# Performance work log

Hardware: AMD Instinct MI355X
Metric: run time of the kernel (lower is better)

Reference implementation:

```python
import jax, jax.numpy as jnp
import numpy as np

EMB_DIM = 512
QKV_DIM = 512
NUM_HEADS = 8
HEAD_DIM = QKV_DIM // NUM_HEADS
NUM_LANDMARKS = 64
N_ITER = 6


def setup_inputs() -> dict:
    key = jax.random.key(0)
    ks = jax.random.split(key, 9)
    s = 1.0 / np.sqrt(EMB_DIM)
    return {
        "x": jax.random.normal(ks[0], (4, 8192, EMB_DIM), dtype=jnp.float32),
        "Wq": jax.random.normal(ks[1], (EMB_DIM, QKV_DIM), dtype=jnp.float32) * s,
        "bq": jnp.zeros((QKV_DIM,), dtype=jnp.float32),
        "Wk": jax.random.normal(ks[2], (EMB_DIM, QKV_DIM), dtype=jnp.float32) * s,
        "bk": jnp.zeros((QKV_DIM,), dtype=jnp.float32),
        "Wv": jax.random.normal(ks[3], (EMB_DIM, QKV_DIM), dtype=jnp.float32) * s,
        "bv": jnp.zeros((QKV_DIM,), dtype=jnp.float32),
        "Wo": jax.random.normal(ks[4], (QKV_DIM, EMB_DIM), dtype=jnp.float32) * s,
        "bo": jnp.zeros((EMB_DIM,), dtype=jnp.float32),
    }


def _split_heads(x):
    bs, sl, _ = x.shape
    return x.reshape(bs, sl, NUM_HEADS, HEAD_DIM).transpose(0, 2, 1, 3)


def _iterative_inv(K):
    # K: [bs, h, L, L]; Newton-Schulz pseudo-inverse, 'original' init
    L = K.shape[-1]
    I = jnp.eye(L, dtype=K.dtype)
    V = K.swapaxes(-1, -2) / jnp.max(jnp.sum(K, axis=-2))
    for _ in range(N_ITER):
        KV = jnp.matmul(K, V)
        V = jnp.matmul(0.25 * V, 13.0 * I - jnp.matmul(KV, 15.0 * I - jnp.matmul(KV, 7.0 * I - KV)))
    return V


def reference(x, Wq, bq, Wk, bk, Wv, bv, Wo, bo):
    bs, seqlen, _ = x.shape
    # seqlen chosen divisible by NUM_LANDMARKS, so no padding branch
    full_len = seqlen
    q = _split_heads(x @ Wq + bq)
    k = _split_heads(x @ Wk + bk)
    v = _split_heads(x @ Wv + bv)
    scale = 1.0 / np.sqrt(np.sqrt(HEAD_DIM))
    q = q * scale
    k = k * scale

    seg = full_len // NUM_LANDMARKS
    q_land = q.reshape(bs, NUM_HEADS, NUM_LANDMARKS, seg, HEAD_DIM).mean(axis=-2)
    k_land = k.reshape(bs, NUM_HEADS, NUM_LANDMARKS, seg, HEAD_DIM).mean(axis=-2)

    kernel_1 = jax.nn.softmax(jnp.einsum('bhsd,bhld->bhsl', q, k_land), axis=-1)  # [bs,h,S,L]
    kernel_2 = jax.nn.softmax(jnp.einsum('bhld,bhmd->bhlm', q_land, k_land), axis=-1)  # [bs,h,L,L]
    kernel_3 = jax.nn.softmax(jnp.einsum('bhld,bhsd->bhls', q_land, k), axis=-1)  # [bs,h,L,S]

    out = jnp.matmul(jnp.matmul(kernel_1, _iterative_inv(kernel_2)), jnp.matmul(kernel_3, v))  # [bs,h,S,d]
    out = out.transpose(0, 2, 1, 3).reshape(bs, seqlen, QKV_DIM)
    return out @ Wo + bo
```

## Files before the change

### kernel.cpp

```cpp
#include <hip/hip_runtime.h>

#define BS 4
#define SEQL 8192
#define EMB 512
#define NH 8
#define HD 64
#define LM 64
#define SEG 128
#define BH (BS*NH)
#define NCH 16
#define CHS (SEQL/NCH)
#define QSCALE 0.35355339059327373f

typedef unsigned short u16;
typedef __bf16 bf16_t;
typedef __attribute__((ext_vector_type(8))) __bf16 bf16x8;
typedef __attribute__((ext_vector_type(4))) float f32x4;

#define MFMA16(a, b, c) __builtin_amdgcn_mfma_f32_16x16x32_bf16((a), (b), (c), 0, 0, 0)

__device__ __forceinline__ float bf2f(u16 u) {
  return __uint_as_float(((unsigned int)u) << 16);
}
__device__ __forceinline__ u16 f2bf(float f) {
  unsigned int u = __float_as_uint(f);
  u += 0x7fffu + ((u >> 16) & 1u);
  return (u16)(u >> 16);
}
__device__ __forceinline__ float load1_any(const void* p, size_t idx, int isf32) {
  return isf32 ? ((const float*)p)[idx] : bf2f(((const u16*)p)[idx]);
}
__device__ __forceinline__ void load4_any(const void* p, size_t idx, int isf32, float* dst) {
  if (isf32) {
    float4 v = *reinterpret_cast<const float4*>((const float*)p + idx);
    dst[0] = v.x; dst[1] = v.y; dst[2] = v.z; dst[3] = v.w;
  } else {
    ushort4 v = *reinterpret_cast<const ushort4*>((const u16*)p + idx);
    dst[0] = bf2f(v.x); dst[1] = bf2f(v.y); dst[2] = bf2f(v.z); dst[3] = bf2f(v.w);
  }
}
__device__ __forceinline__ void ld8_bf(const void* p, size_t idx, int isf32, u16* o) {
  if (isf32) {
    const float* f = (const float*)p + idx;
    float4 a = *reinterpret_cast<const float4*>(f);
    float4 b = *reinterpret_cast<const float4*>(f + 4);
    o[0] = f2bf(a.x); o[1] = f2bf(a.y); o[2] = f2bf(a.z); o[3] = f2bf(a.w);
    o[4] = f2bf(b.x); o[5] = f2bf(b.y); o[6] = f2bf(b.z); o[7] = f2bf(b.w);
  } else {
    *reinterpret_cast<int4*>(o) = *reinterpret_cast<const int4*>((const u16*)p + idx);
  }
}

__device__ __forceinline__ void async16(const void* g, void* l) {
  __builtin_amdgcn_global_load_lds(
      (const __attribute__((address_space(1))) void*)g,
      (__attribute__((address_space(3))) void*)l, 16, 0, 0);
}

__global__ __launch_bounds__(256) void probe_kernel(const void* x, int* flag) {
  __shared__ int cnt;
  if (threadIdx.x == 0) cnt = 0;
  __syncthreads();
  const u16* p = (const u16*)x;
  int c = 0;
  for (int j = 0; j < 16; j++) {
    u16 u = p[(size_t)(threadIdx.x * 16 + j) * 2];
    int e = (u >> 7) & 0xFF;
    if (e >= 134) c++;
  }
  atomicAdd(&cnt, c);
  __syncthreads();
  if (threadIdx.x == 0) flag[0] = (cnt > 256) ? 1 : 0;
}

__global__ __launch_bounds__(256) void prep_wt_kernel(
    const void* Wq, const void* Wk, const void* Wv, const void* Wo, const int* flag,
    u16* __restrict__ WqT, u16* __restrict__ WkT, u16* __restrict__ WvT, u16* __restrict__ WoT)
{
  __shared__ u16 Ws[64 * 72];
  const int id = blockIdx.x;
  const int z = id >> 6, tile = id & 63;
  const int k0 = (tile >> 3) * 64, n0 = (tile & 7) * 64;
  const void* W = (z == 0) ? Wq : (z == 1) ? Wk : (z == 2) ? Wv : Wo;
  u16* WT = (z == 0) ? WqT : (z == 1) ? WkT : (z == 2) ? WvT : WoT;
  const int isf32 = flag[0];
  const int t = threadIdx.x;
  const int r = t >> 2, cq = (t & 3) * 16;
  u16 tmp[8];
  #pragma unroll
  for (int u = 0; u < 2; u++) {
    ld8_bf(W, (size_t)(k0 + r) * EMB + n0 + cq + 8 * u, isf32, tmp);
    *reinterpret_cast<int4*>(&Ws[r * 72 + cq + 8 * u]) = *reinterpret_cast<int4*>(tmp);
  }
  __syncthreads();
  const int nn = t >> 2, kq = (t & 3) * 16;
  #pragma unroll
  for (int u = 0; u < 2; u++) {
    u16 o[8];
    #pragma unroll
    for (int j = 0; j < 8; j++) o[j] = Ws[(kq + 8 * u + j) * 72 + nn];
    *reinterpret_cast<int4*>(&WT[(size_t)(n0 + nn) * EMB + k0 + kq + 8 * u]) =
        *reinterpret_cast<int4*>(o);
  }
}

__global__ __launch_bounds__(256) void xmean_kernel(const void* x, const int* flag,
                                                    float* __restrict__ xmean) {
  const int bl = blockIdx.x;
  const int t = threadIdx.x;
  const int isf32 = flag[0];
  const int c = t * 2;
  const size_t base = (size_t)bl * SEG * EMB;
  float s0 = 0.f, s1 = 0.f;
  for (int r = 0; r < SEG; r++) {
    size_t idx = base + (size_t)r * EMB + c;
    if (isf32) {
      float2 v = *reinterpret_cast<const float2*>((const float*)x + idx);
      s0 += v.x; s1 += v.y;
    } else {
      ushort2 v = *reinterpret_cast<const ushort2*>((const u16*)x + idx);
      s0 += bf2f(v.x); s1 += bf2f(v.y);
    }
  }
  xmean[(size_t)bl * EMB + c]     = s0 * (1.0f / SEG);
  xmean[(size_t)bl * EMB + c + 1] = s1 * (1.0f / SEG);
}

__global__ __launch_bounds__(256) void lm_proj_kernel(
    const float* __restrict__ xmean,
    const void* Wq, const void* bq, const void* Wk, const void* bk,
    const int* flag, float* __restrict__ qL, float* __restrict__ kL,
    u16* __restrict__ qLb, u16* __restrict__ kLb)
{
  __shared__ float As[64 * 17];
  __shared__ float Bs[16 * 64];
  const int t = threadIdx.x;
  const int m0 = blockIdx.x * 64, n0 = blockIdx.y * 64, z = blockIdx.z;
  const void* W    = z ? Wk : Wq;
  const void* bias = z ? bk : bq;
  float* dst       = z ? kL : qL;
  u16*   dstb      = z ? kLb : qLb;
  const int isf32 = flag[0];
  const int tx = t & 15, ty = t >> 4;
  const int arow = t >> 2, akk = (t & 3) << 2;
  const int brow = t >> 4, bcol = (t & 15) << 2;
  float acc[4][4] = {};
  for (int k0 = 0; k0 < EMB; k0 += 16) {
    float4 av = *reinterpret_cast<const float4*>(xmean + (size_t)(m0 + arow) * EMB + k0 + akk);
    As[arow * 17 + akk + 0] = av.x;
    As[arow * 17 + akk + 1] = av.y;
    As[arow * 17 + akk + 2] = av.z;
    As[arow * 17 + akk + 3] = av.w;
    load4_any(W, (size_t)(k0 + brow) * EMB + n0 + bcol, isf32, &Bs[brow * 64 + bcol]);
    __syncthreads();
    #pragma unroll
    for (int kk = 0; kk < 16; kk++) {
      float a[4], b[4];
      #pragma unroll
      for (int i = 0; i < 4; i++) a[i] = As[(ty * 4 + i) * 17 + kk];
      #pragma unroll
      for (int j = 0; j < 4; j++) b[j] = Bs[kk * 64 + tx * 4 + j];
      #pragma unroll
      for (int i = 0; i < 4; i++)
        #pragma unroll
        for (int j = 0; j < 4; j++)
          acc[i][j] = fmaf(a[i], b[j], acc[i][j]);
    }
    __syncthreads();
  }
  #pragma unroll
  for (int i = 0; i < 4; i++) {
    int m = m0 + ty * 4 + i;
    int b = m >> 6, l = m & 63;
    #pragma unroll
    for (int j = 0; j < 4; j++) {
      int n = n0 + tx * 4 + j;
      int h = n >> 6, d = n & 63;
      float c = (acc[i][j] + load1_any(bias, n, isf32)) * QSCALE;
      size_t idx = (size_t)((b * NH + h) * LM + l) * HD + d;
      dst[idx] = c;
      dstb[idx] = f2bf(c);
    }
  }
}

__global__ __launch_bounds__(256, 3) void proj_qkv_fused_kernel(
    const void* x, const u16* __restrict__ WqT, const u16* __restrict__ WkT,
    const u16* __restrict__ WvT,
    const void* bq, const void* bk, const void* bv, const int* flag,
    u16* __restrict__ Qb, u16* __restrict__ Kb, u16* __restrict__ VbT)
{
  __shared__ u16 smem[128 * 72 + 3 * 64 * 64];
  u16* As = smem;
  u16* Bs = smem + 128 * 72;
  const int t = threadIdx.x;
  const int orig = blockIdx.x;
  const int swz  = (orig & 7) * 256 + (orig >> 3);
  const int h    = swz & 7;
  const int m0   = (swz >> 3) * 128;
  const int n0   = h * 64;
  const int isf32 = flag[0];
  const int w = t >> 6, lane = t & 63, q = lane >> 4, c = lane & 15;
  const int wm = (w >> 1) * 64, wn = (w & 1) * 32;
  const int sr = t >> 1, sh = (t & 1) * 32;
  const int brow8 = lane >> 3;
  const int bsw   = ((lane & 7) ^ brow8) * 8;

  f32x4 acc[3][4][2];
  f32x4 z4 = {0.f, 0.f, 0.f, 0.f};
  #pragma unroll
  for (int z = 0; z < 3; z++)
    #pragma unroll
    for (int mi = 0; mi < 4; mi++) { acc[z][mi][0] = z4; acc[z][mi][1] = z4; }

  for (int k0 = 0; k0 < EMB; k0 += 64) {
    __syncthreads();
    #pragma unroll
    for (int u = 0; u < 6; u++) {
      int cb = u * 4 + w;
      int z = cb >> 3, r8 = cb & 7;
      const u16* Wt = (z == 0) ? WqT : (z == 1) ? WkT : WvT;
      async16(&Wt[(size_t)(n0 + r8 * 8 + brow8) * EMB + k0 + bsw],
              &Bs[z * 4096 + r8 * 512]);
    }
    u16 tmp[8];
    #pragma unroll
    for (int u = 0; u < 4; u++) {
      ld8_bf(x, (size_t)(m0 + sr) * EMB + k0 + sh + 8 * u, isf32, tmp);
      *reinterpret_cast<int4*>(&As[sr * 72 + sh + 8 * u]) = *reinterpret_cast<int4*>(tmp);
    }
    __syncthreads();
    #pragma unroll
    for (int kk = 0; kk < 64; kk += 32) {
      bf16x8 af[4];
      #pragma unroll
      for (int mi = 0; mi < 4; mi++)
        af[mi] = *reinterpret_cast<const bf16x8*>(&As[(wm + mi * 16 + c) * 72 + kk + q * 8]);
      const int u0 = ((((kk >> 3) + q) ^ (c & 7))) * 8;
      #pragma unroll
      for (int z = 0; z < 3; z++) {
        bf16x8 b0 = *reinterpret_cast<const bf16x8*>(&Bs[z * 4096 + (wn + c) * 64 + u0]);
        bf16x8 b1 = *reinterpret_cast<const bf16x8*>(&Bs[z * 4096 + (wn + 16 + c) * 64 + u0]);
        #pragma unroll
        for (int mi = 0; mi < 4; mi++) {
          acc[z][mi][0] = MFMA16(af[mi], b0, acc[z][mi][0]);
          acc[z][mi][1] = MFMA16(af[mi], b1, acc[z][mi][1]);
        }
      }
    }
  }

  float bb[3][2];
  #pragma unroll
  for (int z = 0; z < 3; z++) {
    const void* bias = (z == 0) ? bq : (z == 1) ? bk : bv;
    bb[z][0] = load1_any(bias, n0 + wn + c, isf32);
    bb[z][1] = load1_any(bias, n0 + wn + 16 + c, isf32);
  }
  const int b = m0 >> 13, s0t = m0 & (SEQL - 1);

  #pragma unroll
  for (int z = 0; z < 2; z++) {
    u16* dst = z ? Kb : Qb;
    #pragma unroll
    for (int mi = 0; mi < 4; mi++)
      #pragma unroll
      for (int i = 0; i < 4; i++) {
        int s = s0t + wm + mi * 16 + q * 4 + i;
        size_t rowb = ((size_t)((b * NH + h) * SEQL + s)) * HD;
        dst[rowb + wn + c]      = f2bf((acc[z][mi][0][i] + bb[z][0]) * QSCALE);
        dst[rowb + wn + 16 + c] = f2bf((acc[z][mi][1][i] + bb[z][1]) * QSCALE);
      }
  }

  __syncthreads();
  #pragma unroll
  for (int mi = 0; mi < 4; mi++)
    #pragma unroll
    for (int i = 0; i < 4; i++) {
      int ml = wm + mi * 16 + q * 4 + i;
      smem[(wn + c) * 136 + ml]      = f2bf(acc[2][mi][0][i] + bb[2][0]);
      smem[(wn + 16 + c) * 136 + ml] = f2bf(acc[2][mi][1][i] + bb[2][1]);
    }
  __syncthreads();
  const int nl = t >> 2, cq2 = (t & 3) * 32;
  #pragma unroll
  for (int u = 0; u < 4; u++)
    *reinterpret_cast<int4*>(&VbT[((size_t)((b * NH + h) * HD + nl)) * SEQL + s0t + cq2 + 8 * u]) =
        *reinterpret_cast<int4*>(&smem[nl * 136 + cq2 + 8 * u]);
}

__global__ __launch_bounds__(256) void k2_softmax_kernel(
    const float* __restrict__ qL, const float* __restrict__ kL,
    float* __restrict__ K2, float* __restrict__ cs)
{
  __shared__ float qs[64 * 65], ks[64 * 65], ps[64 * 65];
  const int t = threadIdx.x, bh = blockIdx.x;
  const int r = t >> 2, cb = (t & 3) << 4;
  #pragma unroll
  for (int i = 0; i < 16; i++) {
    qs[r * 65 + cb + i] = qL[((size_t)bh * LM + r) * HD + cb + i];
    ks[r * 65 + cb + i] = kL[((size_t)bh * LM + r) * HD + cb + i];
  }
  __syncthreads();
  float lg[16] = {};
  for (int d = 0; d < HD; d++) {
    float a = qs[r * 65 + d];
    #pragma unroll
    for (int i = 0; i < 16; i++) lg[i] = fmaf(a, ks[(cb + i) * 65 + d], lg[i]);
  }
  float m = lg[0];
  #pragma unroll
  for (int i = 1; i < 16; i++) m = fmaxf(m, lg[i]);
  m = fmaxf(m, __shfl_xor(m, 1));
  m = fmaxf(m, __shfl_xor(m, 2));
  float s = 0.f;
  #pragma unroll
  for (int i = 0; i < 16; i++) { lg[i] = __expf(lg[i] - m); s += lg[i]; }
  s += __shfl_xor(s, 1);
  s += __shfl_xor(s, 2);
  const float inv = 1.0f / s;
  #pragma unroll
  for (int i = 0; i < 16; i++) {
    float p = lg[i] * inv;
    ps[r * 65 + cb + i] = p;
    K2[((size_t)bh * LM + r) * LM + cb + i] = p;
  }
  __syncthreads();
  if (t < 64) {
    float c = 0.f;
    for (int rr = 0; rr < 64; rr++) c += ps[rr * 65 + t];
    cs[bh * LM + t] = c;
  }
}

__device__ __forceinline__ void mm_split(const u16* Ah, const u16* Al,
                                         const u16* Bh, const u16* Bl,
                                         int w, int lane, f32x4* out)
{
  const int q = lane >> 4, c = lane & 15;
  bf16x8 ah[2], al[2];
  #pragma unroll
  for (int k2 = 0; k2 < 2; k2++) {
    ah[k2] = *reinterpret_cast<const bf16x8*>(&Ah[(w * 16 + c) * 72 + k2 * 32 + q * 8]);
    al[k2] = *reinterpret_cast<const bf16x8*>(&Al[(w * 16 + c) * 72 + k2 * 32 + q * 8]);
  }
  #pragma unroll
  for (int nb = 0; nb < 4; nb++) {
    f32x4 acc = {0.f, 0.f, 0.f, 0.f};
    #pragma unroll
    for (int k2 = 0; k2 < 2; k2++) {
      bf16x8 bh_ = *reinterpret_cast<const bf16x8*>(&Bh[(nb * 16 + c) * 72 + k2 * 32 + q * 8]);
      bf16x8 bl_ = *reinterpret_cast<const bf16x8*>(&Bl[(nb * 16 + c) * 72 + k2 * 32 + q * 8]);
      acc = MFMA16(ah[k2], bh_, acc);
      acc = MFMA16(ah[k2], bl_, acc);
      acc = MFMA16(al[k2], bh_, acc);
    }
    out[nb] = acc;
  }
}

__global__ __launch_bounds__(256) void ns_inverse_kernel(
    const float* __restrict__ K2, const float* __restrict__ cs,
    float* __restrict__ Vi)
{
  __shared__ u16 K2h[64 * 72], K2l[64 * 72];
  __shared__ u16 VAh[64 * 72], VAl[64 * 72];
  __shared__ u16 VTh[64 * 72], VTl[64 * 72];
  __shared__ u16 KVh[64 * 72], KVl[64 * 72];
  __shared__ u16 Th [64 * 72], Tl [64 * 72];
  __shared__ float red[256];
  const int t = threadIdx.x, bh = blockIdx.x;
  const int w = t >> 6, lane = t & 63, q = lane >> 4, c = lane & 15;

  float m = -1e30f;
  for (int i = t; i < BH * LM; i += 256) m = fmaxf(m, cs[i]);
  red[t] = m;
  __syncthreads();
  for (int off = 128; off; off >>= 1) {
    if (t < off) red[t] = fmaxf(red[t], red[t + off]);
    __syncthreads();
  }
  const float ginv = 1.0f / red[0];
  __syncthreads();

  {
    const int r = t >> 2, cb = (t & 3) << 4;
    #pragma unroll
    for (int i = 0; i < 16; i++) {
      float v = K2[((size_t)bh * LM + r) * LM + cb + i];
      u16 h1 = f2bf(v);
      K2h[r * 72 + cb + i] = h1;
      K2l[r * 72 + cb + i] = f2bf(v - bf2f(h1));
      float sv = v * ginv;
      u16 h2 = f2bf(sv);
      u16 l2 = f2bf(sv - bf2f(h2));
      VTh[r * 72 + cb + i] = h2;
      VTl[r * 72 + cb + i] = l2;
      VAh[(cb + i) * 72 + r] = h2;
      VAl[(cb + i) * 72 + r] = l2;
    }
  }
  __syncthreads();

  f32x4 o[4];
  for (int it = 0; it < 6; it++) {
    mm_split(K2h, K2l, VTh, VTl, w, lane, o);
    __syncthreads();
    #pragma unroll
    for (int nb = 0; nb < 4; nb++)
      #pragma unroll
      for (int i = 0; i < 4; i++) {
        const int row = w * 16 + q * 4 + i, col = nb * 16 + c;
        const float v = o[nb][i];
        const u16 h1 = f2bf(v);
        KVh[row * 72 + col] = h1;
        KVl[row * 72 + col] = f2bf(v - bf2f(h1));
        const float tv = (row == col ? 7.0f : 0.0f) - v;
        const u16 h2 = f2bf(tv);
        Th[col * 72 + row] = h2;
        Tl[col * 72 + row] = f2bf(tv - bf2f(h2));
      }
    __syncthreads();
    mm_split(KVh, KVl, Th, Tl, w, lane, o);
    __syncthreads();
    #pragma unroll
    for (int nb = 0; nb < 4; nb++)
      #pragma unroll
      for (int i = 0; i < 4; i++) {
        const int row = w * 16 + q * 4 + i, col = nb * 16 + c;
        const float tv = (row == col ? 15.0f : 0.0f) - o[nb][i];
        const u16 h2 = f2bf(tv);
        Th[col * 72 + row] = h2;
        Tl[col * 72 + row] = f2bf(tv - bf2f(h2));
      }
    __syncthreads();
    mm_split(KVh, KVl, Th, Tl, w, lane, o);
    __syncthreads();
    #pragma unroll
    for (int nb = 0; nb < 4; nb++)
      #pragma unroll
      for (int i = 0; i < 4; i++) {
        const int row = w * 16 + q * 4 + i, col = nb * 16 + c;
        const float tv = (row == col ? 13.0f : 0.0f) - o[nb][i];
        const u16 h2 = f2bf(tv);
        Th[col * 72 + row] = h2;
        Tl[col * 72 + row] = f2bf(tv - bf2f(h2));
      }
    __syncthreads();
    mm_split(VAh, VAl, Th, Tl, w, lane, o);
    __syncthreads();
    #pragma unroll
    for (int nb = 0; nb < 4; nb++)
      #pragma unroll
      for (int i = 0; i < 4; i++) {
        const int row = w * 16 + q * 4 + i, col = nb * 16 + c;
        const float v = 0.25f * o[nb][i];
        const u16 h1 = f2bf(v);
        const u16 l1 = f2bf(v - bf2f(h1));
        VAh[row * 72 + col] = h1;
        VAl[row * 72 + col] = l1;
        VTh[col * 72 + row] = h1;
        VTl[col * 72 + row] = l1;
        if (it == 5) Vi[((size_t)bh * LM + row) * LM + col] = v;
      }
    __syncthreads();
  }
}

__global__ __launch_bounds__(256) void k3v_kernel(
    const u16* __restrict__ qLb, const u16* __restrict__ Kb, const u16* __restrict__ VbT,
    float* __restrict__ pnum, float* __restrict__ pden)
{
  __shared__ u16 Ks[64 * 72], Vs[64 * 72], Ps[64 * 72];
  __shared__ float denL[256];
  const int t = threadIdx.x, ch = blockIdx.x, bh = blockIdx.y;
  const int w = t >> 6, lane = t & 63, q = lane >> 4, c = lane & 15;
  const int sr = t >> 2, sp = (t & 3) * 16;

  bf16x8 aq[4][2];
  #pragma unroll
  for (int mi = 0; mi < 4; mi++)
    #pragma unroll
    for (int k2 = 0; k2 < 2; k2++)
      aq[mi][k2] = *reinterpret_cast<const bf16x8*>(
          &qLb[((size_t)bh * LM + mi * 16 + c) * HD + k2 * 32 + q * 8]);

  f32x4 z4 = {0.f, 0.f, 0.f, 0.f};
  f32x4 nacc[4];
  #pragma unroll
  for (int mi = 0; mi < 4; mi++) nacc[mi] = z4;
  float denr[16] = {};

  for (int sub = 0; sub < 8; sub++) {
    const int s0 = ch * CHS + sub * 64;
    __syncthreads();
    #pragma unroll
    for (int u = 0; u < 2; u++) {
      *reinterpret_cast<int4*>(&Ks[sr * 72 + sp + 8 * u]) =
          *reinterpret_cast<const int4*>(&Kb[((size_t)bh * SEQL + s0 + sr) * HD + sp + 8 * u]);
      *reinterpret_cast<int4*>(&Vs[sr * 72 + sp + 8 * u]) =
          *reinterpret_cast<const int4*>(&VbT[((size_t)(bh * HD + sr)) * SEQL + s0 + sp + 8 * u]);
    }
    __syncthreads();
    f32x4 sacc[4];
    #pragma unroll
    for (int mi = 0; mi < 4; mi++) sacc[mi] = z4;
    bf16x8 bk0 = *reinterpret_cast<const bf16x8*>(&Ks[(w * 16 + c) * 72 + q * 8]);
    bf16x8 bk1 = *reinterpret_cast<const bf16x8*>(&Ks[(w * 16 + c) * 72 + 32 + q * 8]);
    #pragma unroll
    for (int mi = 0; mi < 4; mi++) {
      sacc[mi] = MFMA16(aq[mi][0], bk0, sacc[mi]);
      sacc[mi] = MFMA16(aq[mi][1], bk1, sacc[mi]);
    }
    #pragma unroll
    for (int mi = 0; mi < 4; mi++)
      #pragma unroll
      for (int i = 0; i < 4; i++) {
        float p = __expf(sacc[mi][i]);
        denr[mi * 4 + i] += p;
        Ps[(mi * 16 + q * 4 + i) * 72 + w * 16 + c] = f2bf(p);
      }
    __syncthreads();
    #pragma unroll
    for (int k2 = 0; k2 < 2; k2++) {
      bf16x8 bv_ = *reinterpret_cast<const bf16x8*>(&Vs[(w * 16 + c) * 72 + k2 * 32 + q * 8]);
      #pragma unroll
      for (int mi = 0; mi < 4; mi++) {
        bf16x8 ap = *reinterpret_cast<const bf16x8*>(&Ps[(mi * 16 + c) * 72 + k2 * 32 + q * 8]);
        nacc[mi] = MFMA16(ap, bv_, nacc[mi]);
      }
    }
  }
  #pragma unroll
  for (int mi = 0; mi < 4; mi++)
    #pragma unroll
    for (int i = 0; i < 4; i++)
      pnum[(((size_t)bh * NCH + ch) * LM + mi * 16 + q * 4 + i) * HD + w * 16 + c] = nacc[mi][i];
  #pragma unroll
  for (int v = 0; v < 16; v++) {
    denr[v] += __shfl_xor(denr[v], 1);
    denr[v] += __shfl_xor(denr[v], 2);
    denr[v] += __shfl_xor(denr[v], 4);
    denr[v] += __shfl_xor(denr[v], 8);
  }
  if (c == 0) {
    #pragma unroll
    for (int mi = 0; mi < 4; mi++)
      #pragma unroll
      for (int i = 0; i < 4; i++)
        denL[w * 64 + mi * 16 + q * 4 + i] = denr[mi * 4 + i];
  }
  __syncthreads();
  if (t < 64)
    pden[((size_t)bh * NCH + ch) * LM + t] = denL[t] + denL[64 + t] + denL[128 + t] + denL[192 + t];
}

__global__ __launch_bounds__(256) void k3v_w2_kernel(
    const float* __restrict__ pnum, const float* __restrict__ pden,
    const float* __restrict__ Vi, u16* __restrict__ W2T)
{
  __shared__ float Vs[64 * 65], Ms[64 * 65], den[64];
  const int t = threadIdx.x, bh = blockIdx.x;
  const int r = t >> 2, cb = (t & 3) << 4;
  #pragma unroll
  for (int i = 0; i < 16; i++) Vs[r * 65 + cb + i] = Vi[((size_t)bh * LM + r) * LM + cb + i];
  float acc[16] = {};
  for (int ch = 0; ch < NCH; ch++) {
    const float* p = pnum + (((size_t)bh * NCH + ch) * LM + r) * HD + cb;
    #pragma unroll
    for (int i = 0; i < 16; i++) acc[i] += p[i];
  }
  if ((t & 3) == 0) {
    float d = 0.f;
    for (int ch = 0; ch < NCH; ch++) d += pden[((size_t)bh * NCH + ch) * LM + r];
    den[r] = d;
  }
  __syncthreads();
  const float dinv = 1.0f / den[r];
  #pragma unroll
  for (int i = 0; i < 16; i++) Ms[r * 65 + cb + i] = acc[i] * dinv;
  __syncthreads();
  float o[16] = {};
  for (int k = 0; k < 64; k++) {
    float a = Vs[r * 65 + k];
    #pragma unroll
    for (int i = 0; i < 16; i++) o[i] = fmaf(a, Ms[k * 65 + cb + i], o[i]);
  }
  #pragma unroll
  for (int i = 0; i < 16; i++)
    W2T[((size_t)bh * HD + cb + i) * LM + r] = f2bf(o[i]);
}

__global__ __launch_bounds__(256) void final_kernel(
    const u16* __restrict__ Qb, const u16* __restrict__ kLb, const u16* __restrict__ W2T,
    u16* __restrict__ pre)
{
  __shared__ u16 Ps[64 * 72];
  __shared__ float mxL[256], smL[256];
  const int t = threadIdx.x, st = blockIdx.x, bh = blockIdx.y;
  const int w = t >> 6, lane = t & 63, q = lane >> 4, c = lane & 15;
  const int sb = st * 64;

  bf16x8 aq[4][2], bkL[2], bw2[2];
  #pragma unroll
  for (int mi = 0; mi < 4; mi++)
    #pragma unroll
    for (int k2 = 0; k2 < 2; k2++)
      aq[mi][k2] = *reinterpret_cast<const bf16x8*>(
          &Qb[((size_t)bh * SEQL + sb + mi * 16 + c) * HD + k2 * 32 + q * 8]);
  #pragma unroll
  for (int k2 = 0; k2 < 2; k2++) {
    bkL[k2] = *reinterpret_cast<const bf16x8*>(
        &kLb[((size_t)bh * LM + w * 16 + c) * HD + k2 * 32 + q * 8]);
    bw2[k2] = *reinterpret_cast<const bf16x8*>(
        &W2T[((size_t)bh * HD + w * 16 + c) * LM + k2 * 32 + q * 8]);
  }

  f32x4 z4 = {0.f, 0.f, 0.f, 0.f};
  f32x4 sacc[4];
  #pragma unroll
  for (int mi = 0; mi < 4; mi++) sacc[mi] = z4;
  #pragma unroll
  for (int k2 = 0; k2 < 2; k2++)
    #pragma unroll
    for (int mi = 0; mi < 4; mi++)
      sacc[mi] = MFMA16(aq[mi][k2], bkL[k2], sacc[mi]);

  float mx[16];
  #pragma unroll
  for (int v = 0; v < 16; v++) {
    mx[v] = sacc[v >> 2][v & 3];
    mx[v] = fmaxf(mx[v], __shfl_xor(mx[v], 1));
    mx[v] = fmaxf(mx[v], __shfl_xor(mx[v], 2));
    mx[v] = fmaxf(mx[v], __shfl_xor(mx[v], 4));
    mx[v] = fmaxf(mx[v], __shfl_xor(mx[v], 8));
  }
  if (c == 0) {
    #pragma unroll
    for (int mi = 0; mi < 4; mi++)
      #pragma unroll
      for (int i = 0; i < 4; i++)
        mxL[w * 64 + mi * 16 + q * 4 + i] = mx[mi * 4 + i];
  }
  __syncthreads();
  float p[16], dn[16];
  #pragma unroll
  for (int mi = 0; mi < 4; mi++)
    #pragma unroll
    for (int i = 0; i < 4; i++) {
      int row = mi * 16 + q * 4 + i;
      float M = fmaxf(fmaxf(mxL[row], mxL[64 + row]), fmaxf(mxL[128 + row], mxL[192 + row]));
      float pp = __expf(sacc[mi][i] - M);
      p[mi * 4 + i] = pp;
      dn[mi * 4 + i] = pp;
    }
  #pragma unroll
  for (int v = 0; v < 16; v++) {
    dn[v] += __shfl_xor(dn[v], 1);
    dn[v] += __shfl_xor(dn[v], 2);
    dn[v] += __shfl_xor(dn[v], 4);
    dn[v] += __shfl_xor(dn[v], 8);
  }
  if (c == 0) {
    #pragma unroll
    for (int mi = 0; mi < 4; mi++)
      #pragma unroll
      for (int i = 0; i < 4; i++)
        smL[w * 64 + mi * 16 + q * 4 + i] = dn[mi * 4 + i];
  }
  #pragma unroll
  for (int mi = 0; mi < 4; mi++)
    #pragma unroll
    for (int i = 0; i < 4; i++)
      Ps[(mi * 16 + q * 4 + i) * 72 + w * 16 + c] = f2bf(p[mi * 4 + i]);
  __syncthreads();

  f32x4 oacc[4];
  #pragma unroll
  for (int mi = 0; mi < 4; mi++) oacc[mi] = z4;
  #pragma unroll
  for (int k2 = 0; k2 < 2; k2++)
    #pragma unroll
    for (int mi = 0; mi < 4; mi++) {
      bf16x8 ap = *reinterpret_cast<const bf16x8*>(&Ps[(mi * 16 + c) * 72 + k2 * 32 + q * 8]);
      oacc[mi] = MFMA16(ap, bw2[k2], oacc[mi]);
    }
  #pragma unroll
  for (int mi = 0; mi < 4; mi++)
    #pragma unroll
    for (int i = 0; i < 4; i++) {
      int row = mi * 16 + q * 4 + i;
      float den = smL[row] + smL[64 + row] + smL[128 + row] + smL[192 + row];
      float v = oacc[mi][i] / den;
      pre[((size_t)((bh >> 3) * SEQL + sb + row)) * EMB + (bh & 7) * HD + w * 16 + c] = f2bf(v);
    }
}

__global__ __launch_bounds__(256, 3) void out_proj_kernel(
    const u16* __restrict__ pre, const u16* __restrict__ WoT, const void* bo,
    const int* flag, void* out)
{
  __shared__ u16 As[128 * 64];
  __shared__ u16 Bs[128 * 64];
  const int t = threadIdx.x;
  const int m0 = blockIdx.x * 128, n0 = blockIdx.y * 128;
  const int isf32 = flag[0];
  const int w = t >> 6, lane = t & 63, q = lane >> 4, c = lane & 15;
  const int wm = (w >> 1) * 64, wn = (w & 1) * 64;
  const int row8 = lane >> 3;
  const int colsw = ((lane & 7) ^ row8) * 8;

  f32x4 acc[4][4];
  f32x4 z4 = {0.f, 0.f, 0.f, 0.f};
  #pragma unroll
  for (int mi = 0; mi < 4; mi++)
    #pragma unroll
    for (int ni = 0; ni < 4; ni++) acc[mi][ni] = z4;

  for (int k0 = 0; k0 < EMB; k0 += 64) {
    __syncthreads();
    #pragma unroll
    for (int u = 0; u < 4; u++) {
      int chA = u * 4 + w;
      async16(&pre[(size_t)(m0 + chA * 8 + row8) * EMB + k0 + colsw], &As[chA * 512]);
      async16(&WoT[(size_t)(n0 + chA * 8 + row8) * EMB + k0 + colsw], &Bs[chA * 512]);
    }
    __syncthreads();
    #pragma unroll
    for (int kk = 0; kk < 64; kk += 32) {
      const int u0 = ((((kk >> 3) + q) ^ (c & 7))) * 8;
      bf16x8 af[4], bfv[4];
      #pragma unroll
      for (int mi = 0; mi < 4; mi++)
        af[mi] = *reinterpret_cast<const bf16x8*>(&As[(wm + mi * 16 + c) * 64 + u0]);
      #pragma unroll
      for (int ni = 0; ni < 4; ni++)
        bfv[ni] = *reinterpret_cast<const bf16x8*>(&Bs[(wn + ni * 16 + c) * 64 + u0]);
      #pragma unroll
      for (int mi = 0; mi < 4; mi++)
        #pragma unroll
        for (int ni = 0; ni < 4; ni++)
          acc[mi][ni] = MFMA16(af[mi], bfv[ni], acc[mi][ni]);
    }
  }
  float bb[4];
  #pragma unroll
  for (int ni = 0; ni < 4; ni++) bb[ni] = load1_any(bo, n0 + wn + ni * 16 + c, isf32);
  #pragma unroll
  for (int mi = 0; mi < 4; mi++)
    #pragma unroll
    for (int i = 0; i < 4; i++) {
      int m = m0 + wm + mi * 16 + q * 4 + i;
      #pragma unroll
      for (int ni = 0; ni < 4; ni++) {
        int n = n0 + wn + ni * 16 + c;
        float v = acc[mi][ni][i] + bb[ni];
        if (isf32) ((float*)out)[(size_t)m * EMB + n] = v;
        else       ((u16*)out)[(size_t)m * EMB + n] = f2bf(v);
      }
    }
}

extern "C" void kernel_launch(void* const* d_in, const int* in_sizes, int n_in,
                              void* d_out, int out_size, void* d_ws, size_t ws_size,
                              hipStream_t stream)
{
  (void)in_sizes; (void)n_in; (void)out_size; (void)ws_size;
  const void* x  = d_in[0];
  const void* Wq = d_in[1];
  const void* bq = d_in[2];
  const void* Wk = d_in[3];
  const void* bk = d_in[4];
  const void* Wv = d_in[5];
  const void* bv = d_in[6];
  const void* Wo = d_in[7];
  const void* bo = d_in[8];

  float* ws = (float*)d_ws;
  int*   flag  = (int*)ws;
  float* xmean = ws + 64;
  float* qL    = xmean + 131072;
  float* kL    = qL + 131072;
  float* K2    = kL + 131072;
  float* cs    = K2 + 131072;
  float* Vi    = cs + 2048;
  float* pnum  = Vi + 131072;
  float* pden  = pnum + 2097152;
  u16* WqT = (u16*)(pden + 32768);
  u16* WkT = WqT + 262144;
  u16* WvT = WkT + 262144;
  u16* WoT = WvT + 262144;
  u16* qLb = WoT + 262144;
  u16* kLb = qLb + 131072;
  u16* W2T = kLb + 131072;
  u16* Qb  = W2T + 131072;
  u16* Kb  = Qb + 16777216;
  u16* VbT = Kb + 16777216;
  u16* pre = Kb;

  probe_kernel<<<1, 256, 0, stream>>>(x, flag);
  prep_wt_kernel<<<256, 256, 0, stream>>>(Wq, Wk, Wv, Wo, flag, WqT, WkT, WvT, WoT);
  xmean_kernel<<<BS * LM, 256, 0, stream>>>(x, flag, xmean);
  lm_proj_kernel<<<dim3(4, 8, 2), 256, 0, stream>>>(xmean, Wq, bq, Wk, bk, flag, qL, kL, qLb, kLb);
  proj_qkv_fused_kernel<<<dim3(2048), 256, 0, stream>>>(
      x, WqT, WkT, WvT, bq, bk, bv, flag, Qb, Kb, VbT);
  k2_softmax_kernel<<<BH, 256, 0, stream>>>(qL, kL, K2, cs);
  ns_inverse_kernel<<<BH, 256, 0, stream>>>(K2, cs, Vi);
  k3v_kernel<<<dim3(NCH, BH), 256, 0, stream>>>(qLb, Kb, VbT, pnum, pden);
  k3v_w2_kernel<<<BH, 256, 0, stream>>>(pnum, pden, Vi, W2T);
  final_kernel<<<dim3(SEQL / 64, BH), 256, 0, stream>>>(Qb, kLb, W2T, pre);
  out_proj_kernel<<<dim3(256, 4), 256, 0, stream>>>(pre, WoT, bo, flag, d_out);
}
```

Before: 421.9 us.

## Double-buffer LDS tiles in QKV projection, out-projection and k3v kernels

Adds double-buffered LDS staging to the fused QKV projection and the output projection. The next K-tile's global loads (async global-to-LDS for the weights, register prefetch for x) are issued before the MFMA work on the current tile, which removes one barrier per iteration. The x tile in LDS switches from padded rows to an XOR-swizzled layout. In k3v, the next K/V chunk is prefetched into registers and V gets two LDS buffers. The cost is more LDS per block and lower launch-bound occupancy (3 to 2 blocks per CU) in the two GEMM kernels.

```diff
diff --git a/kernel.cpp b/kernel.cpp
--- a/kernel.cpp
+++ b/kernel.cpp
@@ -55,6 +55,39 @@
   __builtin_amdgcn_global_load_lds(
       (const __attribute__((address_space(1))) void*)g,
       (__attribute__((address_space(3))) void*)l, 16, 0, 0);
+}
+
+struct XRegs {
+  float4 xf[8];
+  int4   xb[4];
+};
+__device__ __forceinline__ void loadx(const void* x, size_t base, int isf32, XRegs& r) {
+  if (isf32) {
+    const float* xp = (const float*)x + base;
+    #pragma unroll
+    for (int u = 0; u < 8; u++) r.xf[u] = *reinterpret_cast<const float4*>(xp + u * 4);
+  } else {
+    const u16* xp = (const u16*)x + base;
+    #pragma unroll
+    for (int u = 0; u < 4; u++) r.xb[u] = *reinterpret_cast<const int4*>(xp + u * 8);
+  }
+}
+__device__ __forceinline__ void writea(u16* As, int dst, int sr, int b0u, int isf32, XRegs& r) {
+  #pragma unroll
+  for (int u = 0; u < 4; u++) {
+    u16 tmp[8];
+    if (isf32) {
+      tmp[0] = f2bf(r.xf[2*u].x); tmp[1] = f2bf(r.xf[2*u].y);
+      tmp[2] = f2bf(r.xf[2*u].z); tmp[3] = f2bf(r.xf[2*u].w);
+      tmp[4] = f2bf(r.xf[2*u+1].x); tmp[5] = f2bf(r.xf[2*u+1].y);
+      tmp[6] = f2bf(r.xf[2*u+1].z); tmp[7] = f2bf(r.xf[2*u+1].w);
+    } else {
+      *reinterpret_cast<int4*>(tmp) = r.xb[u];
+    }
+    const int us = (b0u + u) ^ (sr & 7);
+    *reinterpret_cast<int4*>(&As[dst * 8192 + sr * 64 + us * 8]) =
+        *reinterpret_cast<int4*>(tmp);
+  }
 }
 
 __global__ __launch_bounds__(256) void probe_kernel(const void* x, int* flag) {
@@ -184,15 +217,15 @@
   }
 }
 
-__global__ __launch_bounds__(256, 3) void proj_qkv_fused_kernel(
+__global__ __launch_bounds__(256, 2) void proj_qkv_fused_kernel(
     const void* x, const u16* __restrict__ WqT, const u16* __restrict__ WkT,
     const u16* __restrict__ WvT,
     const void* bq, const void* bk, const void* bv, const int* flag,
     u16* __restrict__ Qb, u16* __restrict__ Kb, u16* __restrict__ VbT)
 {
-  __shared__ u16 smem[128 * 72 + 3 * 64 * 64];
+  __shared__ u16 smem[2 * 128 * 64 + 2 * 3 * 64 * 64];
   u16* As = smem;
-  u16* Bs = smem + 128 * 72;
+  u16* Bs = smem + 2 * 128 * 64;
   const int t = threadIdx.x;
   const int orig = blockIdx.x;
   const int swz  = (orig & 7) * 256 + (orig >> 3);
@@ -202,7 +235,7 @@
   const int isf32 = flag[0];
   const int w = t >> 6, lane = t & 63, q = lane >> 4, c = lane & 15;
   const int wm = (w >> 1) * 64, wn = (w & 1) * 32;
-  const int sr = t >> 1, sh = (t & 1) * 32;
+  const int sr = t >> 1, b0u = (t & 1) * 4;
   const int brow8 = lane >> 3;
   const int bsw   = ((lane & 7) ^ brow8) * 8;
 
@@ -213,41 +246,56 @@
     #pragma unroll
     for (int mi = 0; mi < 4; mi++) { acc[z][mi][0] = z4; acc[z][mi][1] = z4; }
 
-  for (int k0 = 0; k0 < EMB; k0 += 64) {
-    __syncthreads();
-    #pragma unroll
-    for (int u = 0; u < 6; u++) {
-      int cb = u * 4 + w;
-      int z = cb >> 3, r8 = cb & 7;
-      const u16* Wt = (z == 0) ? WqT : (z == 1) ? WkT : WvT;
-      async16(&Wt[(size_t)(n0 + r8 * 8 + brow8) * EMB + k0 + bsw],
-              &Bs[z * 4096 + r8 * 512]);
-    }
-    u16 tmp[8];
-    #pragma unroll
-    for (int u = 0; u < 4; u++) {
-      ld8_bf(x, (size_t)(m0 + sr) * EMB + k0 + sh + 8 * u, isf32, tmp);
-      *reinterpret_cast<int4*>(&As[sr * 72 + sh + 8 * u]) = *reinterpret_cast<int4*>(tmp);
-    }
-    __syncthreads();
+  XRegs xr;
+  const size_t xrow = (size_t)(m0 + sr) * EMB + b0u * 8;
+
+  loadx(x, xrow + 0, isf32, xr);
+  #pragma unroll
+  for (int u = 0; u < 6; u++) {
+    int cb = u * 4 + w, z = cb >> 3, r8 = cb & 7;
+    const u16* Wt = (z == 0) ? WqT : (z == 1) ? WkT : WvT;
+    async16(&Wt[(size_t)(n0 + r8 * 8 + brow8) * EMB + 0 + bsw],
+            &Bs[0 * 12288 + z * 4096 + r8 * 512]);
+  }
+  writea(As, 0, sr, b0u, isf32, xr);
+  __syncthreads();
+
+  for (int tt = 0; tt < 8; tt++) {
+    const int cur = tt & 1;
+    if (tt < 7) {
+      const int k1 = (tt + 1) * 64;
+      loadx(x, xrow + k1, isf32, xr);
+      #pragma unroll
+      for (int u = 0; u < 6; u++) {
+        int cb = u * 4 + w, z = cb >> 3, r8 = cb & 7;
+        const u16* Wt = (z == 0) ? WqT : (z == 1) ? WkT : WvT;
+        async16(&Wt[(size_t)(n0 + r8 * 8 + brow8) * EMB + k1 + bsw],
+                &Bs[(cur ^ 1) * 12288 + z * 4096 + r8 * 512]);
+      }
+    }
     #pragma unroll
     for (int kk = 0; kk < 64; kk += 32) {
+      const int u0 = ((((kk >> 3) + q) ^ (c & 7))) * 8;
       bf16x8 af[4];
       #pragma unroll
       for (int mi = 0; mi < 4; mi++)
-        af[mi] = *reinterpret_cast<const bf16x8*>(&As[(wm + mi * 16 + c) * 72 + kk + q * 8]);
-      const int u0 = ((((kk >> 3) + q) ^ (c & 7))) * 8;
+        af[mi] = *reinterpret_cast<const bf16x8*>(
+            &As[cur * 8192 + (wm + mi * 16 + c) * 64 + u0]);
       #pragma unroll
       for (int z = 0; z < 3; z++) {
-        bf16x8 b0 = *reinterpret_cast<const bf16x8*>(&Bs[z * 4096 + (wn + c) * 64 + u0]);
-        bf16x8 b1 = *reinterpret_cast<const bf16x8*>(&Bs[z * 4096 + (wn + 16 + c) * 64 + u0]);
+        bf16x8 b0v = *reinterpret_cast<const bf16x8*>(
+            &Bs[cur * 12288 + z * 4096 + (wn + c) * 64 + u0]);
+        bf16x8 b1v = *reinterpret_cast<const bf16x8*>(
+            &Bs[cur * 12288 + z * 4096 + (wn + 16 + c) * 64 + u0]);
         #pragma unroll
         for (int mi = 0; mi < 4; mi++) {
-          acc[z][mi][0] = MFMA16(af[mi], b0, acc[z][mi][0]);
-          acc[z][mi][1] = MFMA16(af[mi], b1, acc[z][mi][1]);
+          acc[z][mi][0] = MFMA16(af[mi], b0v, acc[z][mi][0]);
+          acc[z][mi][1] = MFMA16(af[mi], b1v, acc[z][mi][1]);
         }
       }
     }
+    if (tt < 7) writea(As, cur ^ 1, sr, b0u, isf32, xr);
+    __syncthreads();
   }
 
   float bb[3][2];
@@ -472,7 +520,7 @@
     const u16* __restrict__ qLb, const u16* __restrict__ Kb, const u16* __restrict__ VbT,
     float* __restrict__ pnum, float* __restrict__ pden)
 {
-  __shared__ u16 Ks[64 * 72], Vs[64 * 72], Ps[64 * 72];
+  __shared__ u16 Ks[64 * 72], Vs[2][64 * 72], Ps[64 * 72];
   __shared__ float denL[256];
   const int t = threadIdx.x, ch = blockIdx.x, bh = blockIdx.y;
   const int w = t >> 6, lane = t & 63, q = lane >> 4, c = lane & 15;
@@ -492,16 +540,23 @@
   for (int mi = 0; mi < 4; mi++) nacc[mi] = z4;
   float denr[16] = {};
 
+  int4 kr0, kr1, vr0, vr1;
+  {
+    const int s0 = ch * CHS;
+    const u16* kp = &Kb[((size_t)bh * SEQL + s0 + sr) * HD + sp];
+    const u16* vp = &VbT[((size_t)(bh * HD + sr)) * SEQL + s0 + sp];
+    kr0 = *reinterpret_cast<const int4*>(kp);
+    kr1 = *reinterpret_cast<const int4*>(kp + 8);
+    vr0 = *reinterpret_cast<const int4*>(vp);
+    vr1 = *reinterpret_cast<const int4*>(vp + 8);
+  }
+
   for (int sub = 0; sub < 8; sub++) {
-    const int s0 = ch * CHS + sub * 64;
-    __syncthreads();
-    #pragma unroll
-    for (int u = 0; u < 2; u++) {
-      *reinterpret_cast<int4*>(&Ks[sr * 72 + sp + 8 * u]) =
-          *reinterpret_cast<const int4*>(&Kb[((size_t)bh * SEQL + s0 + sr) * HD + sp + 8 * u]);
-      *reinterpret_cast<int4*>(&Vs[sr * 72 + sp + 8 * u]) =
-          *reinterpret_cast<const int4*>(&VbT[((size_t)(bh * HD + sr)) * SEQL + s0 + sp + 8 * u]);
-    }
+    const int cur = sub & 1;
+    *reinterpret_cast<int4*>(&Ks[sr * 72 + sp])     = kr0;
+    *reinterpret_cast<int4*>(&Ks[sr * 72 + sp + 8]) = kr1;
+    *reinterpret_cast<int4*>(&Vs[cur][sr * 72 + sp])     = vr0;
+    *reinterpret_cast<int4*>(&Vs[cur][sr * 72 + sp + 8]) = vr1;
     __syncthreads();
     f32x4 sacc[4];
     #pragma unroll
@@ -522,9 +577,18 @@
         Ps[(mi * 16 + q * 4 + i) * 72 + w * 16 + c] = f2bf(p);
       }
     __syncthreads();
+    if (sub < 7) {
+      const int s1 = ch * CHS + (sub + 1) * 64;
+      const u16* kp = &Kb[((size_t)bh * SEQL + s1 + sr) * HD + sp];
+      const u16* vp = &VbT[((size_t)(bh * HD + sr)) * SEQL + s1 + sp];
+      kr0 = *reinterpret_cast<const int4*>(kp);
+      kr1 = *reinterpret_cast<const int4*>(kp + 8);
+      vr0 = *reinterpret_cast<const int4*>(vp);
+      vr1 = *reinterpret_cast<const int4*>(vp + 8);
+    }
     #pragma unroll
     for (int k2 = 0; k2 < 2; k2++) {
-      bf16x8 bv_ = *reinterpret_cast<const bf16x8*>(&Vs[(w * 16 + c) * 72 + k2 * 32 + q * 8]);
+      bf16x8 bv_ = *reinterpret_cast<const bf16x8*>(&Vs[cur][(w * 16 + c) * 72 + k2 * 32 + q * 8]);
       #pragma unroll
       for (int mi = 0; mi < 4; mi++) {
         bf16x8 ap = *reinterpret_cast<const bf16x8*>(&Ps[(mi * 16 + c) * 72 + k2 * 32 + q * 8]);
@@ -697,12 +761,12 @@
     }
 }
 
-__global__ __launch_bounds__(256, 3) void out_proj_kernel(
+__global__ __launch_bounds__(256, 2) void out_proj_kernel(
     const u16* __restrict__ pre, const u16* __restrict__ WoT, const void* bo,
     const int* flag, void* out)
 {
-  __shared__ u16 As[128 * 64];
-  __shared__ u16 Bs[128 * 64];
+  __shared__ u16 As[2 * 128 * 64];
+  __shared__ u16 Bs[2 * 128 * 64];
   const int t = threadIdx.x;
   const int m0 = blockIdx.x * 128, n0 = blockIdx.y * 128;
   const int isf32 = flag[0];
@@ -718,31 +782,44 @@
     #pragma unroll
     for (int ni = 0; ni < 4; ni++) acc[mi][ni] = z4;
 
-  for (int k0 = 0; k0 < EMB; k0 += 64) {
-    __syncthreads();
-    #pragma unroll
-    for (int u = 0; u < 4; u++) {
-      int chA = u * 4 + w;
-      async16(&pre[(size_t)(m0 + chA * 8 + row8) * EMB + k0 + colsw], &As[chA * 512]);
-      async16(&WoT[(size_t)(n0 + chA * 8 + row8) * EMB + k0 + colsw], &Bs[chA * 512]);
-    }
-    __syncthreads();
+  #pragma unroll
+  for (int u = 0; u < 4; u++) {
+    int chA = u * 4 + w;
+    async16(&pre[(size_t)(m0 + chA * 8 + row8) * EMB + 0 + colsw], &As[chA * 512]);
+    async16(&WoT[(size_t)(n0 + chA * 8 + row8) * EMB + 0 + colsw], &Bs[chA * 512]);
+  }
+  __syncthreads();
+
+  for (int tt = 0; tt < 8; tt++) {
+    const int cur = tt & 1;
+    if (tt < 7) {
+      const int k1 = (tt + 1) * 64;
+      #pragma unroll
+      for (int u = 0; u < 4; u++) {
+        int chA = u * 4 + w;
+        async16(&pre[(size_t)(m0 + chA * 8 + row8) * EMB + k1 + colsw],
+                &As[(cur ^ 1) * 8192 + chA * 512]);
+        async16(&WoT[(size_t)(n0 + chA * 8 + row8) * EMB + k1 + colsw],
+                &Bs[(cur ^ 1) * 8192 + chA * 512]);
+      }
+    }
     #pragma unroll
     for (int kk = 0; kk < 64; kk += 32) {
       const int u0 = ((((kk >> 3) + q) ^ (c & 7))) * 8;
       bf16x8 af[4], bfv[4];
       #pragma unroll
       for (int mi = 0; mi < 4; mi++)
-        af[mi] = *reinterpret_cast<const bf16x8*>(&As[(wm + mi * 16 + c) * 64 + u0]);
+        af[mi] = *reinterpret_cast<const bf16x8*>(&As[cur * 8192 + (wm + mi * 16 + c) * 64 + u0]);
       #pragma unroll
       for (int ni = 0; ni < 4; ni++)
-        bfv[ni] = *reinterpret_cast<const bf16x8*>(&Bs[(wn + ni * 16 + c) * 64 + u0]);
+        bfv[ni] = *reinterpret_cast<const bf16x8*>(&Bs[cur * 8192 + (wn + ni * 16 + c) * 64 + u0]);
       #pragma unroll
       for (int mi = 0; mi < 4; mi++)
         #pragma unroll
         for (int ni = 0; ni < 4; ni++)
           acc[mi][ni] = MFMA16(af[mi], bfv[ni], acc[mi][ni]);
     }
+    __syncthreads();
   }
   float bb[4];
   #pragma unroll
```

Result: slower. 528.9 us (+25.4%).
